# Kernel optimization log

Hardware: AMD Instinct MI355X
Metric: run time of the kernel (lower is better)

## Reference

```python
import jax, jax.numpy as jnp
import numpy as np

NUM_TYPES = 8
IN_FEATURES = 1024
OUT_FEATURES = 1024
N = 65536


def setup_inputs() -> dict:
    key = jax.random.key(0)
    k_x, k_t, k_w, k_b = jax.random.split(key, 4)
    x = jax.random.normal(k_x, (N, IN_FEATURES), dtype=jnp.float32)
    types = jnp.sort(jax.random.randint(k_t, (N,), 0, NUM_TYPES, dtype=jnp.int32))
    # Per-type Linear params; PyTorch Linear stores weight as [out, in] and
    # computes x @ W.T + b. We store W as [T, in, out] (pre-transposed).
    bound = 1.0 / np.sqrt(IN_FEATURES)
    W = jax.random.uniform(k_w, (NUM_TYPES, IN_FEATURES, OUT_FEATURES), dtype=jnp.float32,
                           minval=-bound, maxval=bound)
    b = jax.random.uniform(k_b, (NUM_TYPES, OUT_FEATURES), dtype=jnp.float32,
                           minval=-bound, maxval=bound)
    return {"x": x, "types": types, "W": W, "b": b}


def reference(x, types, W, b):
    # out[n] = x[n] @ W[types[n]] + b[types[n]]
    # Small fixed loop over num_types: one masked GEMM per type (grouped GEMM).
    num_types = W.shape[0]
    out = jnp.zeros((x.shape[0], W.shape[2]), dtype=x.dtype)
    for t in range(num_types):
        mask = (types == t)[:, None]  # [N, 1]
        out = out + jnp.where(mask, x @ W[t] + b[t], 0.0)
    return out
```

## Files before the change

kernel.cpp:

```cpp
#include <hip/hip_runtime.h>
#include <hip/hip_bf16.h>

#define NROWS 65536
#define KDIM  1024
#define NOUT  1024
#define NTYPE 8

typedef __attribute__((ext_vector_type(8))) short bf16x8;
typedef __attribute__((ext_vector_type(4))) float f32x4;

__device__ __forceinline__ unsigned int pk2_rn(float a, float b) {
  unsigned int ua = __float_as_uint(a);
  unsigned int ub = __float_as_uint(b);
  ua += 0x7fffu + ((ua >> 16) & 1u);
  ub += 0x7fffu + ((ub >> 16) & 1u);
  return (ua >> 16) | (ub & 0xffff0000u);
}

__device__ __forceinline__ void async_cp16(const void* g, void* l) {
  __builtin_amdgcn_global_load_lds(
      (const __attribute__((address_space(1))) unsigned int*)g,
      (__attribute__((address_space(3))) unsigned int*)l, 16, 0, 0);
}

__global__ void wtrans_kernel(const float* __restrict__ W,
                              unsigned short* __restrict__ Wt) {
  const int ty    = blockIdx.x;
  const int ntile = blockIdx.y;
  const int ks    = blockIdx.z;
  const int n   = ntile * 64 + (threadIdx.x >> 2);
  const int kcs = threadIdx.x & 3;
  const float* src = W + (size_t)ty * (KDIM * NOUT);
  unsigned short* dst = Wt + (size_t)ty * (KDIM * NOUT);
  const int sw = (n >> 1) & 3;
  for (int round = 0; round < 8; ++round) {
    int kc = ks * 32 + round * 4 + kcs;
    int k0 = kc * 8;
    float v[8];
#pragma unroll
    for (int j = 0; j < 8; ++j) v[j] = src[(size_t)(k0 + j) * NOUT + n];
    uint4 o;
    o.x = pk2_rn(v[0], v[1]);
    o.y = pk2_rn(v[2], v[3]);
    o.z = pk2_rn(v[4], v[5]);
    o.w = pk2_rn(v[6], v[7]);
    int G  = kc >> 2;
    int bp = (kc & 3) ^ sw;
    *(uint4*)(dst + (size_t)n * KDIM + G * 32 + bp * 8) = o;
  }
}

__global__ __launch_bounds__(256) void typed_gemm_kernel(
    const float* __restrict__ x, const int* __restrict__ types,
    const unsigned short* __restrict__ Wt, const float* __restrict__ bias,
    float* __restrict__ out) {
  __shared__ unsigned short As[128 * 32];
  __shared__ unsigned short Bs[128 * 32];

  const int tid  = threadIdx.x;
  const int lane = tid & 63;
  const int wave = tid >> 6;
  const int quad = lane >> 4;
  const int l16  = lane & 15;

  const int n0 = blockIdx.x * 128;
  const int m0 = blockIdx.y * 128;

  const int t0 = types[m0];
  const int t1 = types[m0 + 127];
  const bool multi = (t0 != t1);

  int srow[4], stype[4], aoff[4];
  const float* agp[4];
#pragma unroll
  for (int r = 0; r < 4; ++r) {
    int idx = r * 256 + tid;
    int m = idx >> 3;
    int kc = idx & 7;
    srow[r]  = m;
    stype[r] = types[m0 + m];
    int b  = kc >> 1;
    int h  = kc & 1;
    int bp = b ^ ((m >> 1) & 3);
    aoff[r] = m * 32 + bp * 8 + h * 4;
    agp[r]  = x + (size_t)(m0 + m) * KDIM + kc * 4;
  }

  const int mbase = (wave & 1) * 64;
  const int nbase = (wave >> 1) * 64;

  int ard[4], brd[4];
#pragma unroll
  for (int mt = 0; mt < 4; ++mt) {
    int m = mbase + mt * 16 + l16;
    ard[mt] = m * 32 + (quad ^ ((m >> 1) & 3)) * 8;
  }
#pragma unroll
  for (int nt = 0; nt < 4; ++nt) {
    int n = nbase + nt * 16 + l16;
    brd[nt] = n * 32 + (quad ^ ((n >> 1) & 3)) * 8;
  }

  f32x4 acc[4][4];
#pragma unroll
  for (int i = 0; i < 4; ++i)
#pragma unroll
    for (int j = 0; j < 4; ++j) acc[i][j] = (f32x4){0.f, 0.f, 0.f, 0.f};

  const int brow = lane >> 2;
  const int bchk = lane & 3;

  for (int t = t0; t <= t1; ++t) {
    const unsigned short* wbase = Wt + (size_t)t * (KDIM * NOUT);
    bool msk[4];
#pragma unroll
    for (int r = 0; r < 4; ++r) msk[r] = (stype[r] == t);

    for (int kb = 0; kb < KDIM; kb += 32) {
      {
        int seg0 = wave * 2;
        int seg1 = seg0 + 1;
        const unsigned short* g0 =
            wbase + (size_t)(n0 + seg0 * 16 + brow) * KDIM + kb + bchk * 8;
        const unsigned short* g1 =
            wbase + (size_t)(n0 + seg1 * 16 + brow) * KDIM + kb + bchk * 8;
        async_cp16(g0, &Bs[seg0 * 512 + lane * 8]);
        async_cp16(g1, &Bs[seg1 * 512 + lane * 8]);
      }
#pragma unroll
      for (int r = 0; r < 4; ++r) {
        float4 v = *(const float4*)(agp[r] + kb);
        uint2 p;
        p.x = pk2_rn(v.x, v.y);
        p.y = pk2_rn(v.z, v.w);
        if (!msk[r]) { p.x = 0u; p.y = 0u; }
        *(uint2*)(&As[aoff[r]]) = p;
      }
      __syncthreads();

      bf16x8 af[4], bfr[4];
#pragma unroll
      for (int i = 0; i < 4; ++i) af[i] = *(const bf16x8*)(&As[ard[i]]);
#pragma unroll
      for (int i = 0; i < 4; ++i) bfr[i] = *(const bf16x8*)(&Bs[brd[i]]);
#pragma unroll
      for (int mt = 0; mt < 4; ++mt)
#pragma unroll
        for (int nt = 0; nt < 4; ++nt)
          acc[mt][nt] = __builtin_amdgcn_mfma_f32_16x16x32_bf16(
              af[mt], bfr[nt], acc[mt][nt], 0, 0, 0);
      __syncthreads();
    }
  }

  float bval[4];
  if (!multi) {
#pragma unroll
    for (int nt = 0; nt < 4; ++nt)
      bval[nt] = bias[t0 * NOUT + n0 + nbase + nt * 16 + l16];
  }
#pragma unroll
  for (int mt = 0; mt < 4; ++mt) {
#pragma unroll
    for (int reg = 0; reg < 4; ++reg) {
      int rl = mbase + mt * 16 + quad * 4 + reg;
      int grow = m0 + rl;
      float* orow = out + (size_t)grow * NOUT + n0 + nbase + l16;
      if (!multi) {
#pragma unroll
        for (int nt = 0; nt < 4; ++nt)
          orow[nt * 16] = acc[mt][nt][reg] + bval[nt];
      } else {
        int ty = types[grow];
#pragma unroll
        for (int nt = 0; nt < 4; ++nt)
          orow[nt * 16] =
              acc[mt][nt][reg] + bias[ty * NOUT + n0 + nbase + nt * 16 + l16];
      }
    }
  }
}

extern "C" void kernel_launch(void* const* d_in, const int* in_sizes, int n_in,
                              void* d_out, int out_size, void* d_ws,
                              size_t ws_size, hipStream_t stream) {
  const float* x     = (const float*)d_in[0];
  const int*   types = (const int*)d_in[1];
  const float* W     = (const float*)d_in[2];
  const float* b     = (const float*)d_in[3];
  float* out = (float*)d_out;
  unsigned short* Wt = (unsigned short*)d_ws;

  wtrans_kernel<<<dim3(NTYPE, 16, 4), 256, 0, stream>>>(W, Wt);
  typed_gemm_kernel<<<dim3(NOUT / 128, NROWS / 128), 256, 0, stream>>>(
      x, types, Wt, b, out);
}
```

Baseline: 688.0 us.

## Double-buffer GEMM LDS stages, remap blocks per XCD, tile weight transpose via LDS

The typed GEMM main loop now uses two LDS buffers. The next k-slice's global loads (x in registers, W via async LDS copy) are issued before the MFMAs on the current slice, and one barrier per step replaces two. The type loop and k loop are flattened into a single stage counter. Workgroup indices are remapped so each XCD handles a contiguous band of M rows across all N tiles, improving L2 reuse of x. The weight transpose kernel now goes through an LDS tile so its global reads and writes coalesce. The costs are twice the LDS footprint and added register pressure from the prefetched x values.

```diff
diff --git a/kernel.cpp b/kernel.cpp
--- a/kernel.cpp
+++ b/kernel.cpp
@@ -23,30 +23,44 @@
       (__attribute__((address_space(3))) unsigned int*)l, 16, 0, 0);
 }
 
-__global__ void wtrans_kernel(const float* __restrict__ W,
-                              unsigned short* __restrict__ Wt) {
-  const int ty    = blockIdx.x;
-  const int ntile = blockIdx.y;
-  const int ks    = blockIdx.z;
-  const int n   = ntile * 64 + (threadIdx.x >> 2);
-  const int kcs = threadIdx.x & 3;
+__global__ __launch_bounds__(256) void wtrans_kernel(
+    const float* __restrict__ W, unsigned short* __restrict__ Wt) {
+  __shared__ unsigned short T[64 * 66];
+  unsigned int* Tw = (unsigned int*)T;
+
+  const int ty = blockIdx.x;
+  const int k0 = blockIdx.y * 64;
+  const int n0 = blockIdx.z * 64;
   const float* src = W + (size_t)ty * (KDIM * NOUT);
   unsigned short* dst = Wt + (size_t)ty * (KDIM * NOUT);
-  const int sw = (n >> 1) & 3;
-  for (int round = 0; round < 8; ++round) {
-    int kc = ks * 32 + round * 4 + kcs;
-    int k0 = kc * 8;
-    float v[8];
-#pragma unroll
-    for (int j = 0; j < 8; ++j) v[j] = src[(size_t)(k0 + j) * NOUT + n];
+
+  const int tid = threadIdx.x;
+  const int k2 = tid >> 5;
+  const int n2 = tid & 31;
+
+#pragma unroll
+  for (int p = 0; p < 4; ++p) {
+    int kl = p * 16 + k2 * 2;
+    float2 v0 = *(const float2*)(src + (size_t)(k0 + kl) * NOUT + n0 + n2 * 2);
+    float2 v1 = *(const float2*)(src + (size_t)(k0 + kl + 1) * NOUT + n0 + n2 * 2);
+    Tw[(n2 * 2) * 33 + p * 8 + k2]     = pk2_rn(v0.x, v1.x);
+    Tw[(n2 * 2 + 1) * 33 + p * 8 + k2] = pk2_rn(v0.y, v1.y);
+  }
+  __syncthreads();
+
+  const int c   = tid & 7;
+  const int nl0 = tid >> 3;
+#pragma unroll
+  for (int p = 0; p < 2; ++p) {
+    int nl = nl0 + p * 32;
+    int ng = n0 + nl;
+    const unsigned int* tw = Tw + nl * 33 + c * 4;
     uint4 o;
-    o.x = pk2_rn(v[0], v[1]);
-    o.y = pk2_rn(v[2], v[3]);
-    o.z = pk2_rn(v[4], v[5]);
-    o.w = pk2_rn(v[6], v[7]);
+    o.x = tw[0]; o.y = tw[1]; o.z = tw[2]; o.w = tw[3];
+    int kc = (k0 >> 3) + c;
     int G  = kc >> 2;
-    int bp = (kc & 3) ^ sw;
-    *(uint4*)(dst + (size_t)n * KDIM + G * 32 + bp * 8) = o;
+    int bp = (kc & 3) ^ ((ng >> 1) & 3);
+    *(uint4*)(dst + (size_t)ng * KDIM + G * 32 + bp * 8) = o;
   }
 }
 
@@ -54,8 +68,8 @@
     const float* __restrict__ x, const int* __restrict__ types,
     const unsigned short* __restrict__ Wt, const float* __restrict__ bias,
     float* __restrict__ out) {
-  __shared__ unsigned short As[128 * 32];
-  __shared__ unsigned short Bs[128 * 32];
+  __shared__ unsigned short As[2][128 * 32];
+  __shared__ unsigned short Bs[2][128 * 32];
 
   const int tid  = threadIdx.x;
   const int lane = tid & 63;
@@ -63,21 +77,24 @@
   const int quad = lane >> 4;
   const int l16  = lane & 15;
 
-  const int n0 = blockIdx.x * 128;
-  const int m0 = blockIdx.y * 128;
+  const int wg   = blockIdx.y * gridDim.x + blockIdx.x;
+  const int xcd  = wg & 7;
+  const int idx  = wg >> 3;
+  const int n0   = (idx & 7) * 128;
+  const int m0   = ((xcd << 6) + (idx >> 3)) * 128;
 
   const int t0 = types[m0];
   const int t1 = types[m0 + 127];
   const bool multi = (t0 != t1);
-
-  int srow[4], stype[4], aoff[4];
+  const int S = (t1 - t0 + 1) * 32;
+
+  int stype[4], aoff[4];
   const float* agp[4];
 #pragma unroll
   for (int r = 0; r < 4; ++r) {
-    int idx = r * 256 + tid;
-    int m = idx >> 3;
-    int kc = idx & 7;
-    srow[r]  = m;
+    int idx2 = r * 256 + tid;
+    int m = idx2 >> 3;
+    int kc = idx2 & 7;
     stype[r] = types[m0 + m];
     int b  = kc >> 1;
     int h  = kc & 1;
@@ -110,47 +127,56 @@
   const int brow = lane >> 2;
   const int bchk = lane & 3;
 
-  for (int t = t0; t <= t1; ++t) {
+  float4 av[4];
+
+  auto stage_load = [&](int s, int buf) {
+    const int t  = t0 + (s >> 5);
+    const int kb = (s & 31) << 5;
+#pragma unroll
+    for (int r = 0; r < 4; ++r) av[r] = *(const float4*)(agp[r] + kb);
     const unsigned short* wbase = Wt + (size_t)t * (KDIM * NOUT);
-    bool msk[4];
-#pragma unroll
-    for (int r = 0; r < 4; ++r) msk[r] = (stype[r] == t);
-
-    for (int kb = 0; kb < KDIM; kb += 32) {
-      {
-        int seg0 = wave * 2;
-        int seg1 = seg0 + 1;
-        const unsigned short* g0 =
-            wbase + (size_t)(n0 + seg0 * 16 + brow) * KDIM + kb + bchk * 8;
-        const unsigned short* g1 =
-            wbase + (size_t)(n0 + seg1 * 16 + brow) * KDIM + kb + bchk * 8;
-        async_cp16(g0, &Bs[seg0 * 512 + lane * 8]);
-        async_cp16(g1, &Bs[seg1 * 512 + lane * 8]);
-      }
-#pragma unroll
-      for (int r = 0; r < 4; ++r) {
-        float4 v = *(const float4*)(agp[r] + kb);
-        uint2 p;
-        p.x = pk2_rn(v.x, v.y);
-        p.y = pk2_rn(v.z, v.w);
-        if (!msk[r]) { p.x = 0u; p.y = 0u; }
-        *(uint2*)(&As[aoff[r]]) = p;
-      }
-      __syncthreads();
-
-      bf16x8 af[4], bfr[4];
-#pragma unroll
-      for (int i = 0; i < 4; ++i) af[i] = *(const bf16x8*)(&As[ard[i]]);
-#pragma unroll
-      for (int i = 0; i < 4; ++i) bfr[i] = *(const bf16x8*)(&Bs[brd[i]]);
-#pragma unroll
-      for (int mt = 0; mt < 4; ++mt)
-#pragma unroll
-        for (int nt = 0; nt < 4; ++nt)
-          acc[mt][nt] = __builtin_amdgcn_mfma_f32_16x16x32_bf16(
-              af[mt], bfr[nt], acc[mt][nt], 0, 0, 0);
-      __syncthreads();
+    const int seg0 = wave * 2;
+    const unsigned short* g0 =
+        wbase + (size_t)(n0 + seg0 * 16 + brow) * KDIM + kb + bchk * 8;
+    async_cp16(g0, &Bs[buf][seg0 * 512 + lane * 8]);
+    async_cp16(g0 + (size_t)16 * KDIM, &Bs[buf][(seg0 + 1) * 512 + lane * 8]);
+  };
+
+  auto stage_write = [&](int s, int buf) {
+    const int t = t0 + (s >> 5);
+#pragma unroll
+    for (int r = 0; r < 4; ++r) {
+      uint2 p;
+      p.x = pk2_rn(av[r].x, av[r].y);
+      p.y = pk2_rn(av[r].z, av[r].w);
+      if (stype[r] != t) { p.x = 0u; p.y = 0u; }
+      *(uint2*)(&As[buf][aoff[r]]) = p;
     }
+  };
+
+  stage_load(0, 0);
+  stage_write(0, 0);
+  __syncthreads();
+
+  for (int s = 0; s < S; ++s) {
+    const int cur = s & 1;
+    const int nxt = cur ^ 1;
+    if (s + 1 < S) stage_load(s + 1, nxt);
+
+    bf16x8 af[4], bfr[4];
+#pragma unroll
+    for (int i = 0; i < 4; ++i) af[i] = *(const bf16x8*)(&As[cur][ard[i]]);
+#pragma unroll
+    for (int i = 0; i < 4; ++i) bfr[i] = *(const bf16x8*)(&Bs[cur][brd[i]]);
+#pragma unroll
+    for (int mt = 0; mt < 4; ++mt)
+#pragma unroll
+      for (int nt = 0; nt < 4; ++nt)
+        acc[mt][nt] = __builtin_amdgcn_mfma_f32_16x16x32_bf16(
+            af[mt], bfr[nt], acc[mt][nt], 0, 0, 0);
+
+    if (s + 1 < S) stage_write(s + 1, nxt);
+    __syncthreads();
   }
 
   float bval[4];
@@ -191,7 +217,7 @@
   float* out = (float*)d_out;
   unsigned short* Wt = (unsigned short*)d_ws;
 
-  wtrans_kernel<<<dim3(NTYPE, 16, 4), 256, 0, stream>>>(W, Wt);
+  wtrans_kernel<<<dim3(NTYPE, KDIM / 64, NOUT / 64), 256, 0, stream>>>(W, Wt);
   typed_gemm_kernel<<<dim3(NOUT / 128, NROWS / 128), 256, 0, stream>>>(
       x, types, Wt, b, out);
 }
```

Result: slower. 751.7 us (+9.3%).
